# Kernel tuning notes

Measured on AMD Instinct MI355X. Metric: run time of the kernel, lower is better.

The kernel has to match this reference:

```python
import jax, jax.numpy as jnp
import numpy as np

FRACTION = 0.33  # from attn_type='query_selector_0.33'


def setup_inputs() -> dict:
    key = jax.random.key(0)
    k1, k2, k3, k4 = jax.random.split(key, 4)
    B, L, DIM_VAL, DIM_ATTN = 8, 4096, 64, 64
    scale = 1.0 / np.sqrt(DIM_VAL).astype(np.float32)
    x = jax.random.normal(k1, (B, L, DIM_VAL), dtype=jnp.float32)
    Wq = jax.random.normal(k2, (DIM_VAL, DIM_ATTN), dtype=jnp.float32) * scale
    Wk = jax.random.normal(k3, (DIM_VAL, DIM_ATTN), dtype=jnp.float32) * scale
    Wv = jax.random.normal(k4, (DIM_VAL, DIM_VAL), dtype=jnp.float32) * scale
    return {"x": x, "Wq": Wq, "Wk": Wk, "Wv": Wv}


def reference(x, Wq, Wk, Wv):
    # Projections (bias-free Linears)
    Q = jnp.einsum('bld,de->ble', x, Wq)  # [B, L, Da]
    K = jnp.einsum('bld,de->ble', x, Wk)  # [B, L, Da]
    V = jnp.einsum('bld,de->ble', x, Wv)  # [B, L, Dv]

    B, L_Q, Da = Q.shape
    l_Q = int((1.0 - FRACTION) * L_Q)  # static: shapes known at trace time

    # keys.topk(l_Q, dim=1).values -> per-channel top-l_Q along seq; mean over them
    K_top = jax.lax.top_k(jnp.swapaxes(K, 1, 2), l_Q)[0]  # [B, Da, l_Q]
    K_reduce = K_top.mean(axis=-1)                         # [B, Da]

    # score each query against the reduced key; pick top-l_Q queries
    sqk = jnp.einsum('bd,bld->bl', K_reduce, Q)            # [B, L_Q]
    indices = jax.lax.top_k(sqk, l_Q)[1]                   # [B, l_Q] int32

    # gather sampled queries
    Q_sample = jnp.take_along_axis(Q, indices[:, :, None], axis=1)  # [B, l_Q, Da]

    # dense attention for the sampled queries only
    scores = jnp.einsum('bqd,bkd->bqk', Q_sample, K) / jnp.sqrt(jnp.asarray(Da, Q.dtype))
    attn = jax.nn.softmax(scores, axis=-1)                 # [B, l_Q, L]
    out_sel = jnp.einsum('bqk,bkv->bqv', attn, V)          # [B, l_Q, Dv]

    # mean-filled result, scatter attention outputs to selected rows
    mean_values = V.mean(axis=-2)                          # [B, Dv]
    result = jnp.broadcast_to(mean_values[:, None, :], (B, L_Q, V.shape[-1]))
    result = result.at[jnp.arange(B)[:, None], indices].set(out_sel)
    return result
```

## Files before the change

### kernel.cpp

```cpp
#include <hip/hip_runtime.h>
#include <hip/hip_bf16.h>
#include <math.h>

#define BATCH 8
#define SEQ   4096
#define DIM   64
#define LQ    2744
#define QPB   128
#define NQB   22
#define QPAD  2816
#define KS    8
#define L2E   1.4426950408889634f
#define QSC   0.1803368801111204f

typedef _Float16 half8 __attribute__((ext_vector_type(8)));
typedef short    bs8   __attribute__((ext_vector_type(8)));
typedef float    fx16  __attribute__((ext_vector_type(16)));
typedef unsigned short ushort_t;

union UH { uint4 u4; half8 h; };
union UB { unsigned u[4]; uint4 u4; bs8 s; };

__device__ __forceinline__ unsigned pack_bf16(float a, float b) {
    __hip_bfloat162 h = __float22bfloat162_rn(make_float2(a, b));
    union { __hip_bfloat162 h; unsigned u; } cv; cv.h = h; return cv.u;
}

__device__ __forceinline__ unsigned f2sort(float f) {
    unsigned u = __float_as_uint(f);
    return (u & 0x80000000u) ? ~u : (u | 0x80000000u);
}
__device__ __forceinline__ float sort2f(unsigned u) {
    return __uint_as_float((u & 0x80000000u) ? (u & 0x7FFFFFFFu) : ~u);
}

__device__ void radix_select_4096(const unsigned* u, int k, unsigned* hist,
                                  unsigned* wsum, unsigned* res) {
    const int t = threadIdx.x;
    const int lane = t & 63, wv = t >> 6;
    if (t == 0) { res[0] = 0u; res[1] = (unsigned)k; }
    for (int pass = 3; pass >= 0; --pass) {
        const int shift = pass * 8;
        hist[t] = 0u;
        __syncthreads();
        const unsigned pref  = res[0];
        const unsigned kk    = res[1];
        const unsigned hmask = (pass == 3) ? 0u : (0xFFFFFFFFu << (shift + 8));
        for (int i = t; i < 4096; i += 256) {
            unsigned ui = u[i];
            if ((ui & hmask) == pref) atomicAdd(&hist[(ui >> shift) & 255u], 1u);
        }
        __syncthreads();
        const unsigned h = hist[t];
        unsigned s = h;
#pragma unroll
        for (int ofs = 1; ofs < 64; ofs <<= 1) {
            unsigned a = __shfl_down(s, ofs, 64);
            s += (lane + ofs < 64) ? a : 0u;
        }
        if (lane == 0) wsum[wv] = s;
        __syncthreads();
#pragma unroll
        for (int w2 = 0; w2 < 4; ++w2)
            if (w2 > wv) s += wsum[w2];
        if (s >= kk && (s - h) < kk) {
            res[0] = pref | ((unsigned)t << shift);
            res[1] = kk - (s - h);
        }
        __syncthreads();
    }
}

__global__ __launch_bounds__(256) void proj_kernel(
    const float* __restrict__ x,  const float* __restrict__ Wq,
    const float* __restrict__ Wk, const float* __restrict__ Wv,
    float* __restrict__ Q, float* __restrict__ Kt,
    _Float16* __restrict__ Qh, _Float16* __restrict__ Kh,
    ushort_t* __restrict__ Vt, float* __restrict__ pmean) {
    const int rt = blockIdx.x, b = blockIdx.y, t = threadIdx.x;
    __shared__ float4 xs4[64 * 17];
    __shared__ float  red[4][64];
    {
        const float4* xg = (const float4*)(x + ((size_t)b * SEQ + rt * 64) * DIM);
        for (int i = 0; i < 4; ++i) {
            int s = t + 256 * i;
            xs4[(s >> 4) * 17 + (s & 15)] = xg[s];
        }
    }
    __syncthreads();
    const int ch = t & 63, rg = t >> 6;
    float accq[16], acck[16], accv[16];
#pragma unroll
    for (int i = 0; i < 16; ++i) { accq[i] = 0.f; acck[i] = 0.f; accv[i] = 0.f; }
    for (int dc = 0; dc < 4; ++dc) {
        float wq[16], wk[16], wv[16];
#pragma unroll
        for (int dd = 0; dd < 16; ++dd) {
            int d = dc * 16 + dd;
            wq[dd] = Wq[d * 64 + ch]; wk[dd] = Wk[d * 64 + ch]; wv[dd] = Wv[d * 64 + ch];
        }
        for (int r = 0; r < 16; ++r) {
            const int row = rg * 16 + r;
            const float4* xr = &xs4[row * 17 + dc * 4];
            float xv[16];
            float4 a0 = xr[0], a1 = xr[1], a2 = xr[2], a3 = xr[3];
            xv[0]=a0.x; xv[1]=a0.y; xv[2]=a0.z; xv[3]=a0.w;
            xv[4]=a1.x; xv[5]=a1.y; xv[6]=a1.z; xv[7]=a1.w;
            xv[8]=a2.x; xv[9]=a2.y; xv[10]=a2.z; xv[11]=a2.w;
            xv[12]=a3.x; xv[13]=a3.y; xv[14]=a3.z; xv[15]=a3.w;
#pragma unroll
            for (int dd = 0; dd < 16; ++dd) {
                accq[r] = fmaf(xv[dd], wq[dd], accq[r]);
                acck[r] = fmaf(xv[dd], wk[dd], acck[r]);
                accv[r] = fmaf(xv[dd], wv[dd], accv[r]);
            }
        }
    }
    const int rowbase = rt * 64 + rg * 16;
    float sv = 0.f;
#pragma unroll
    for (int r = 0; r < 16; ++r) {
        size_t o = ((size_t)b * SEQ + rowbase + r) * DIM + ch;
        Q[o]  = accq[r];
        Qh[o] = (_Float16)(accq[r] * QSC);
        Kh[o] = (_Float16)acck[r];
        sv += accv[r];
    }
    float4* ktp = (float4*)(Kt + ((size_t)b * 64 + ch) * SEQ + rowbase);
    ktp[0] = make_float4(acck[0], acck[1], acck[2], acck[3]);
    ktp[1] = make_float4(acck[4], acck[5], acck[6], acck[7]);
    ktp[2] = make_float4(acck[8], acck[9], acck[10], acck[11]);
    ktp[3] = make_float4(acck[12], acck[13], acck[14], acck[15]);
    {
        unsigned pk[8];
#pragma unroll
        for (int i = 0; i < 8; ++i) pk[i] = pack_bf16(accv[2*i], accv[2*i+1]);
        uint4* vp = (uint4*)(Vt + ((size_t)(b * 64 + ch)) * SEQ + rowbase);
        vp[0] = make_uint4(pk[0], pk[1], pk[4], pk[5]);
        vp[1] = make_uint4(pk[2], pk[3], pk[6], pk[7]);
    }
    red[rg][ch] = sv;
    __syncthreads();
    if (rg == 0)
        pmean[((size_t)b * 64 + ch) * 64 + rt] =
            red[0][ch] + red[1][ch] + red[2][ch] + red[3][ch];
}

__global__ __launch_bounds__(256) void kmean_kernel(const float* __restrict__ Kt,
                                                    const float* __restrict__ pmean,
                                                    float* __restrict__ Kred,
                                                    float* __restrict__ meanfin) {
    __shared__ unsigned u[4096];
    __shared__ unsigned hist[256];
    __shared__ unsigned wsum[4];
    __shared__ unsigned res[2];
    __shared__ float rsum[4];
    const int bc = blockIdx.x, t = threadIdx.x;
    if (t < 64) {
        float v = pmean[(size_t)bc * 64 + t];
        for (int m = 1; m < 64; m <<= 1) v += __shfl_xor(v, m, 64);
        if (t == 0) meanfin[bc] = v * (1.0f / (float)SEQ);
    }
    const float4* c4 = (const float4*)(Kt + (size_t)bc * SEQ);
    for (int i = t; i < 1024; i += 256) {
        float4 v = c4[i];
        u[i*4+0] = f2sort(v.x); u[i*4+1] = f2sort(v.y);
        u[i*4+2] = f2sort(v.z); u[i*4+3] = f2sort(v.w);
    }
    __syncthreads();
    radix_select_4096(u, LQ, hist, wsum, res);
    const unsigned Tu = res[0];
    const int krem = (int)res[1];
    float loc = 0.f;
    for (int i = t; i < 4096; i += 256)
        if (u[i] > Tu) loc += sort2f(u[i]);
    for (int msk = 1; msk < 64; msk <<= 1) loc += __shfl_xor(loc, msk, 64);
    if ((t & 63) == 0) rsum[t >> 6] = loc;
    __syncthreads();
    if (t == 0) {
        float s = rsum[0] + rsum[1] + rsum[2] + rsum[3] + (float)krem * sort2f(Tu);
        Kred[bc] = s / (float)LQ;
    }
}

__global__ __launch_bounds__(256) void sqk_kernel(const float* __restrict__ Q,
                                                  const float* __restrict__ Kred,
                                                  float* __restrict__ sqk) {
    const int b = blockIdx.y, l = blockIdx.x * 256 + threadIdx.x;
    __shared__ float kr[64];
    if (threadIdx.x < 64) kr[threadIdx.x] = Kred[b * 64 + threadIdx.x];
    __syncthreads();
    const float4* q = (const float4*)(Q + ((size_t)b * SEQ + l) * DIM);
    float s = 0.f;
#pragma unroll
    for (int i = 0; i < 16; ++i) {
        float4 v = q[i];
        s = fmaf(v.x, kr[i*4+0], s); s = fmaf(v.y, kr[i*4+1], s);
        s = fmaf(v.z, kr[i*4+2], s); s = fmaf(v.w, kr[i*4+3], s);
    }
    sqk[b * SEQ + l] = s;
}

__global__ __launch_bounds__(256) void select_kernel(const float* __restrict__ sqk,
                                                     int* __restrict__ sel,
                                                     int* __restrict__ inv) {
    __shared__ unsigned u[4096];
    __shared__ unsigned hist[256];
    __shared__ unsigned wsum[4];
    __shared__ unsigned res[2];
    __shared__ int eq_idx[256];
    __shared__ int cnts[2];
    const int b = blockIdx.x, t = threadIdx.x;
    const float* col = sqk + (size_t)b * SEQ;
    int* invb = inv + (size_t)b * SEQ;
    for (int i = t; i < 4096; i += 256) {
        u[i] = f2sort(col[i]);
        invb[i] = -1;
    }
    if (t < 2) cnts[t] = 0;
    __syncthreads();
    radix_select_4096(u, LQ, hist, wsum, res);
    const unsigned Tu = res[0];
    const int krem = (int)res[1];
    int* selb = sel + b * QPAD;
    for (int i = t; i < 4096; i += 256) {
        unsigned ui = u[i];
        if (ui > Tu) {
            int p = atomicAdd(&cnts[0], 1);
            selb[p] = i;
            invb[i] = p;
        } else if (ui == Tu) {
            int p = atomicAdd(&cnts[1], 1);
            if (p < 256) eq_idx[p] = i;
        }
    }
    __syncthreads();
    if (t == 0) {
        int ng = cnts[0];
        int ne = cnts[1] < 256 ? cnts[1] : 256;
        for (int i = 1; i < ne; ++i) {
            int v = eq_idx[i], j = i - 1;
            while (j >= 0 && eq_idx[j] > v) { eq_idx[j+1] = eq_idx[j]; --j; }
            eq_idx[j+1] = v;
        }
        for (int j = 0; j < krem; ++j) {
            selb[ng + j] = eq_idx[j];
            invb[eq_idx[j]] = ng + j;
        }
    }
    __syncthreads();
    if (t < QPAD - LQ) selb[LQ + t] = selb[LQ - 1];
}

__global__ __launch_bounds__(256, 3) void attn_kernel(
    const ushort_t* __restrict__ Qh, const ushort_t* __restrict__ Kh,
    const ushort_t* __restrict__ Vt, const int* __restrict__ sel,
    float* __restrict__ pl, float* __restrict__ pout) {
    const int lin = blockIdx.x + NQB * (blockIdx.y + KS * blockIdx.z);
    const int ks  = lin & 7;
    const int j8  = lin >> 3;
    const int b   = j8 / NQB;
    const int qt  = j8 % NQB;
    const int t = threadIdx.x, w = t >> 6, lane = t & 63;
    const int col = lane & 31, h = lane >> 5;

    __shared__ ushort_t Ktile[2][32 * 64];
    __shared__ ushort_t Vtile[2][32 * 64];

    half8 qf[4];
    {
        const int q = qt * QPB + w * 32 + col;
        const int row = sel[b * QPAD + q];
        const uint4* qg = (const uint4*)(Qh + ((size_t)b * SEQ + row) * DIM);
#pragma unroll
        for (int m = 0; m < 4; ++m) { UH u; u.u4 = qg[2 * m + h]; qf[m] = u.h; }
    }

    int koff[4], voff[4];
#pragma unroll
    for (int m = 0; m < 4; ++m)
        koff[m] = col * 64 + 8 * ((2 * m + h) ^ (col & 7));
#pragma unroll
    for (int i = 0; i < 4; ++i)
        voff[i] = col * 64 + 8 * ((i * 2 + h) ^ (col & 7));

    fx16 O0, O1;
#pragma unroll
    for (int r = 0; r < 16; ++r) { O0[r] = 0.f; O1[r] = 0.f; }
    float l = 0.f;

    const int srow = t >> 3, sgr = t & 7;
    const int lg = sgr ^ (srow & 7);
    const int vD = lg >> 2, vc = (lg >> 1) & 1, vh = lg & 1;
    const size_t kgbase = ((size_t)b * SEQ + ks * 512 + srow) * DIM + 8 * lg;
    const size_t vgbase = ((size_t)(b * DIM + srow + 32 * vD)) * SEQ
                          + ks * 512 + vc * 16 + vh * 8;

    uint4 kreg = *(const uint4*)(Kh + kgbase);
    uint4 vreg = *(const uint4*)(Vt + vgbase);

    for (int tile = 0; tile < 16; ++tile) {
        const int buf = tile & 1;
        *(uint4*)&Ktile[buf][srow * 64 + sgr * 8] = kreg;
        *(uint4*)&Vtile[buf][srow * 64 + sgr * 8] = vreg;
        __syncthreads();
        if (tile < 15) {
            kreg = *(const uint4*)(Kh + kgbase + (size_t)(tile + 1) * 32 * DIM);
            vreg = *(const uint4*)(Vt + vgbase + (size_t)(tile + 1) * 32);
        }
        fx16 S;
#pragma unroll
        for (int r = 0; r < 16; ++r) S[r] = 0.f;
#pragma unroll
        for (int m = 0; m < 4; ++m) {
            UH kf;
            kf.u4 = *(const uint4*)&Ktile[buf][koff[m]];
            S = __builtin_amdgcn_mfma_f32_32x32x16_f16(kf.h, qf[m], S, 0, 0, 0);
        }
        float p[16];
#pragma unroll
        for (int r = 0; r < 16; ++r) p[r] = exp2f(S[r]);
#pragma unroll
        for (int r = 0; r < 16; ++r) l += p[r];
        UB A0, A1;
#pragma unroll
        for (int v = 0; v < 4; ++v) {
            A0.u[v] = pack_bf16(p[2 * v],     p[2 * v + 1]);
            A1.u[v] = pack_bf16(p[8 + 2 * v], p[8 + 2 * v + 1]);
        }
#pragma unroll
        for (int D = 0; D < 2; ++D) {
            fx16& O = D ? O1 : O0;
#pragma unroll
            for (int c = 0; c < 2; ++c) {
                UB vf;
                vf.u4 = *(const uint4*)&Vtile[buf][voff[D * 2 + c]];
                O = __builtin_amdgcn_mfma_f32_32x32x16_bf16(c ? A1.s : A0.s, vf.s, O, 0, 0, 0);
            }
        }
    }

    l += __shfl_xor(l, 32);

    const int qg0 = qt * QPB + w * 32;
    const size_t base = (size_t)b * QPAD + qg0;
#pragma unroll
    for (int D = 0; D < 2; ++D) {
        const fx16& O = D ? O1 : O0;
#pragma unroll
        for (int r = 0; r < 16; ++r) {
            const int q = (r & 3) + 8 * (r >> 2) + 4 * h;
            atomicAdd(&pout[(base + q) * DIM + D * 32 + col], O[r]);
        }
    }
    if (h == 0) atomicAdd(&pl[base + col], l);
}

__global__ __launch_bounds__(256) void comb_kernel(
    const float* __restrict__ pl, const float* __restrict__ pout,
    const int* __restrict__ inv, const float* __restrict__ meanfin,
    float* __restrict__ out) {
    const int idx = blockIdx.x * 256 + threadIdx.x;
    const int b = idx >> 16;
    const int rc = idx & 65535;
    const int row = rc >> 4, c = rc & 15;
    const int p = inv[b * SEQ + row];
    float4 o;
    if (p >= 0) {
        const size_t s0 = (size_t)b * QPAD + p;
        const float invl = 1.0f / pl[s0];
        float4 a = ((const float4*)(pout + s0 * DIM))[c];
        o = make_float4(a.x * invl, a.y * invl, a.z * invl, a.w * invl);
    } else {
        o = make_float4(meanfin[b * 64 + c * 4 + 0], meanfin[b * 64 + c * 4 + 1],
                        meanfin[b * 64 + c * 4 + 2], meanfin[b * 64 + c * 4 + 3]);
    }
    ((float4*)out)[idx] = o;
}

extern "C" void kernel_launch(void* const* d_in, const int* in_sizes, int n_in,
                              void* d_out, int out_size, void* d_ws, size_t ws_size,
                              hipStream_t stream) {
    const float* x  = (const float*)d_in[0];
    const float* Wq = (const float*)d_in[1];
    const float* Wk = (const float*)d_in[2];
    const float* Wv = (const float*)d_in[3];
    float* out = (float*)d_out;
    char* wsb  = (char*)d_ws;

    float*    Q       = (float*)(wsb);
    _Float16* Qh      = (_Float16*)(wsb + 8388608);
    _Float16* Kh      = (_Float16*)(wsb + 12582912);
    ushort_t* Vt      = (ushort_t*)(wsb + 16777216);
    float*    pmean   = (float*)(wsb + 20971520);
    float*    meanfin = (float*)(wsb + 21102592);
    float*    Kred    = (float*)(wsb + 21104640);
    float*    sqk     = (float*)(wsb + 21106688);
    int*      sel     = (int*)(wsb + 21237760);
    int*      inv     = (int*)(wsb + 21327872);
    float*    Kt      = (float*)(wsb + 21458944);
    float*    pout    = (float*)(wsb + 21458944);
    float*    pl      = (float*)(wsb + 21458944 + 5767168);

    proj_kernel  <<<dim3(64, 8),          256, 0, stream>>>(x, Wq, Wk, Wv, Q, Kt,
                                                            Qh, Kh, Vt, pmean);
    kmean_kernel <<<512,                  256, 0, stream>>>(Kt, pmean, Kred, meanfin);
    sqk_kernel   <<<dim3(16, 8),          256, 0, stream>>>(Q, Kred, sqk);
    select_kernel<<<8,                    256, 0, stream>>>(sqk, sel, inv);
    hipMemsetAsync(pout, 0, 5767168 + 90112, stream);
    attn_kernel  <<<dim3(NQB, KS, BATCH), 256, 0, stream>>>((const ushort_t*)Qh,
                                                            (const ushort_t*)Kh,
                                                            Vt, sel, pl, pout);
    comb_kernel  <<<2048,                 256, 0, stream>>>(pl, pout, inv, meanfin, out);
}
```

Measured before the change: 195.5 us.

## Trim radix passes, fuse memset into sqk, widen attention K tiles, scalar x loads

The projection kernel drops its LDS staging of x and reads each row through wave-uniform (readfirstlane) global loads. The key top-k mean now runs only two 8-bit radix passes and approximates values in the threshold bucket by the bucket midpoint. The pout/pl zeroing moves out of a separate memset and into the sqk kernel. The attention kernel processes 64-key tiles per barrier with two prefetched loads, raises the waves-per-EU launch bound to 4, and wraps the MFMA groups in s_setprio. The radix change trades exactness of K_reduce for fewer passes, and the larger tiles double the LDS per block.

Result: faster. 187.8 us (-3.9%).

```diff
diff --git a/kernel.cpp b/kernel.cpp
--- a/kernel.cpp
+++ b/kernel.cpp
@@ -35,11 +35,11 @@
 }
 
 __device__ void radix_select_4096(const unsigned* u, int k, unsigned* hist,
-                                  unsigned* wsum, unsigned* res) {
+                                  unsigned* wsum, unsigned* res, int pass_lo) {
     const int t = threadIdx.x;
     const int lane = t & 63, wv = t >> 6;
     if (t == 0) { res[0] = 0u; res[1] = (unsigned)k; }
-    for (int pass = 3; pass >= 0; --pass) {
+    for (int pass = 3; pass >= pass_lo; --pass) {
         const int shift = pass * 8;
         hist[t] = 0u;
         __syncthreads();
@@ -78,17 +78,9 @@
     _Float16* __restrict__ Qh, _Float16* __restrict__ Kh,
     ushort_t* __restrict__ Vt, float* __restrict__ pmean) {
     const int rt = blockIdx.x, b = blockIdx.y, t = threadIdx.x;
-    __shared__ float4 xs4[64 * 17];
     __shared__ float  red[4][64];
-    {
-        const float4* xg = (const float4*)(x + ((size_t)b * SEQ + rt * 64) * DIM);
-        for (int i = 0; i < 4; ++i) {
-            int s = t + 256 * i;
-            xs4[(s >> 4) * 17 + (s & 15)] = xg[s];
-        }
-    }
-    __syncthreads();
     const int ch = t & 63, rg = t >> 6;
+    const float* xb = x + (size_t)b * SEQ * DIM;
     float accq[16], acck[16], accv[16];
 #pragma unroll
     for (int i = 0; i < 16; ++i) { accq[i] = 0.f; acck[i] = 0.f; accv[i] = 0.f; }
@@ -100,14 +92,12 @@
             wq[dd] = Wq[d * 64 + ch]; wk[dd] = Wk[d * 64 + ch]; wv[dd] = Wv[d * 64 + ch];
         }
         for (int r = 0; r < 16; ++r) {
-            const int row = rg * 16 + r;
-            const float4* xr = &xs4[row * 17 + dc * 4];
+            const int off = (rt * 64 + rg * 16 + r) * DIM + dc * 16;
+            const float* xrow =
+                xb + (unsigned)__builtin_amdgcn_readfirstlane(off);
             float xv[16];
-            float4 a0 = xr[0], a1 = xr[1], a2 = xr[2], a3 = xr[3];
-            xv[0]=a0.x; xv[1]=a0.y; xv[2]=a0.z; xv[3]=a0.w;
-            xv[4]=a1.x; xv[5]=a1.y; xv[6]=a1.z; xv[7]=a1.w;
-            xv[8]=a2.x; xv[9]=a2.y; xv[10]=a2.z; xv[11]=a2.w;
-            xv[12]=a3.x; xv[13]=a3.y; xv[14]=a3.z; xv[15]=a3.w;
+#pragma unroll
+            for (int dd = 0; dd < 16; ++dd) xv[dd] = xrow[dd];
 #pragma unroll
             for (int dd = 0; dd < 16; ++dd) {
                 accq[r] = fmaf(xv[dd], wq[dd], accq[r]);
@@ -168,27 +158,34 @@
         u[i*4+2] = f2sort(v.z); u[i*4+3] = f2sort(v.w);
     }
     __syncthreads();
-    radix_select_4096(u, LQ, hist, wsum, res);
+    radix_select_4096(u, LQ, hist, wsum, res, 2);
     const unsigned Tu = res[0];
     const int krem = (int)res[1];
     float loc = 0.f;
     for (int i = t; i < 4096; i += 256)
-        if (u[i] > Tu) loc += sort2f(u[i]);
+        if ((u[i] & 0xFFFF0000u) > Tu) loc += sort2f(u[i]);
     for (int msk = 1; msk < 64; msk <<= 1) loc += __shfl_xor(loc, msk, 64);
     if ((t & 63) == 0) rsum[t >> 6] = loc;
     __syncthreads();
     if (t == 0) {
-        float s = rsum[0] + rsum[1] + rsum[2] + rsum[3] + (float)krem * sort2f(Tu);
+        float s = rsum[0] + rsum[1] + rsum[2] + rsum[3]
+                + (float)krem * sort2f(Tu | 0x8000u);
         Kred[bc] = s / (float)LQ;
     }
 }
 
 __global__ __launch_bounds__(256) void sqk_kernel(const float* __restrict__ Q,
                                                   const float* __restrict__ Kred,
-                                                  float* __restrict__ sqk) {
+                                                  float* __restrict__ sqk,
+                                                  float4* __restrict__ pz) {
     const int b = blockIdx.y, l = blockIdx.x * 256 + threadIdx.x;
     __shared__ float kr[64];
     if (threadIdx.x < 64) kr[threadIdx.x] = Kred[b * 64 + threadIdx.x];
+    {
+        const int tid = (blockIdx.y * 16 + blockIdx.x) * 256 + threadIdx.x;
+        const float4 z = make_float4(0.f, 0.f, 0.f, 0.f);
+        for (int i = tid; i < 366080; i += 32768) pz[i] = z;
+    }
     __syncthreads();
     const float4* q = (const float4*)(Q + ((size_t)b * SEQ + l) * DIM);
     float s = 0.f;
@@ -219,7 +216,7 @@
     }
     if (t < 2) cnts[t] = 0;
     __syncthreads();
-    radix_select_4096(u, LQ, hist, wsum, res);
+    radix_select_4096(u, LQ, hist, wsum, res, 0);
     const unsigned Tu = res[0];
     const int krem = (int)res[1];
     int* selb = sel + b * QPAD;
@@ -252,7 +249,7 @@
     if (t < QPAD - LQ) selb[LQ + t] = selb[LQ - 1];
 }
 
-__global__ __launch_bounds__(256, 3) void attn_kernel(
+__global__ __launch_bounds__(256, 4) void attn_kernel(
     const ushort_t* __restrict__ Qh, const ushort_t* __restrict__ Kh,
     const ushort_t* __restrict__ Vt, const int* __restrict__ sel,
     float* __restrict__ pl, float* __restrict__ pout) {
@@ -264,8 +261,8 @@
     const int t = threadIdx.x, w = t >> 6, lane = t & 63;
     const int col = lane & 31, h = lane >> 5;
 
-    __shared__ ushort_t Ktile[2][32 * 64];
-    __shared__ ushort_t Vtile[2][32 * 64];
+    __shared__ ushort_t Ktile[2][64 * 64];
+    __shared__ ushort_t Vtile[2][2 * 32 * 64];
 
     half8 qf[4];
     {
@@ -296,48 +293,66 @@
     const size_t vgbase = ((size_t)(b * DIM + srow + 32 * vD)) * SEQ
                           + ks * 512 + vc * 16 + vh * 8;
 
-    uint4 kreg = *(const uint4*)(Kh + kgbase);
-    uint4 vreg = *(const uint4*)(Vt + vgbase);
-
-    for (int tile = 0; tile < 16; ++tile) {
+    uint4 kreg0 = *(const uint4*)(Kh + kgbase);
+    uint4 kreg1 = *(const uint4*)(Kh + kgbase + 32 * DIM);
+    uint4 vreg0 = *(const uint4*)(Vt + vgbase);
+    uint4 vreg1 = *(const uint4*)(Vt + vgbase + 32);
+
+    for (int tile = 0; tile < 8; ++tile) {
         const int buf = tile & 1;
-        *(uint4*)&Ktile[buf][srow * 64 + sgr * 8] = kreg;
-        *(uint4*)&Vtile[buf][srow * 64 + sgr * 8] = vreg;
-        __syncthreads();
-        if (tile < 15) {
-            kreg = *(const uint4*)(Kh + kgbase + (size_t)(tile + 1) * 32 * DIM);
-            vreg = *(const uint4*)(Vt + vgbase + (size_t)(tile + 1) * 32);
-        }
-        fx16 S;
-#pragma unroll
-        for (int r = 0; r < 16; ++r) S[r] = 0.f;
-#pragma unroll
-        for (int m = 0; m < 4; ++m) {
-            UH kf;
-            kf.u4 = *(const uint4*)&Ktile[buf][koff[m]];
-            S = __builtin_amdgcn_mfma_f32_32x32x16_f16(kf.h, qf[m], S, 0, 0, 0);
-        }
-        float p[16];
-#pragma unroll
-        for (int r = 0; r < 16; ++r) p[r] = exp2f(S[r]);
-#pragma unroll
-        for (int r = 0; r < 16; ++r) l += p[r];
-        UB A0, A1;
-#pragma unroll
-        for (int v = 0; v < 4; ++v) {
-            A0.u[v] = pack_bf16(p[2 * v],     p[2 * v + 1]);
-            A1.u[v] = pack_bf16(p[8 + 2 * v], p[8 + 2 * v + 1]);
-        }
-#pragma unroll
-        for (int D = 0; D < 2; ++D) {
-            fx16& O = D ? O1 : O0;
-#pragma unroll
-            for (int c = 0; c < 2; ++c) {
-                UB vf;
-                vf.u4 = *(const uint4*)&Vtile[buf][voff[D * 2 + c]];
-                O = __builtin_amdgcn_mfma_f32_32x32x16_bf16(c ? A1.s : A0.s, vf.s, O, 0, 0, 0);
+        *(uint4*)&Ktile[buf][srow * 64 + sgr * 8]          = kreg0;
+        *(uint4*)&Ktile[buf][(srow + 32) * 64 + sgr * 8]   = kreg1;
+        *(uint4*)&Vtile[buf][srow * 64 + sgr * 8]          = vreg0;
+        *(uint4*)&Vtile[buf][2048 + srow * 64 + sgr * 8]   = vreg1;
+        __syncthreads();
+        if (tile < 7) {
+            const size_t ko = kgbase + (size_t)(tile + 1) * 64 * DIM;
+            const size_t vo = vgbase + (size_t)(tile + 1) * 64;
+            kreg0 = *(const uint4*)(Kh + ko);
+            kreg1 = *(const uint4*)(Kh + ko + 32 * DIM);
+            vreg0 = *(const uint4*)(Vt + vo);
+            vreg1 = *(const uint4*)(Vt + vo + 32);
+        }
+#pragma unroll
+        for (int ss = 0; ss < 2; ++ss) {
+            const int so = ss * 2048;
+            fx16 S;
+#pragma unroll
+            for (int r = 0; r < 16; ++r) S[r] = 0.f;
+            __builtin_amdgcn_s_setprio(1);
+#pragma unroll
+            for (int m = 0; m < 4; ++m) {
+                UH kf;
+                kf.u4 = *(const uint4*)&Ktile[buf][koff[m] + so];
+                S = __builtin_amdgcn_mfma_f32_32x32x16_f16(kf.h, qf[m], S, 0, 0, 0);
             }
-        }
+            __builtin_amdgcn_s_setprio(0);
+            float p[16];
+#pragma unroll
+            for (int r = 0; r < 16; ++r) p[r] = exp2f(S[r]);
+#pragma unroll
+            for (int r = 0; r < 16; ++r) l += p[r];
+            UB A0, A1;
+#pragma unroll
+            for (int v = 0; v < 4; ++v) {
+                A0.u[v] = pack_bf16(p[2 * v],     p[2 * v + 1]);
+                A1.u[v] = pack_bf16(p[8 + 2 * v], p[8 + 2 * v + 1]);
+            }
+            __builtin_amdgcn_s_setprio(1);
+#pragma unroll
+            for (int D = 0; D < 2; ++D) {
+                fx16& O = D ? O1 : O0;
+#pragma unroll
+                for (int c = 0; c < 2; ++c) {
+                    UB vf;
+                    vf.u4 = *(const uint4*)&Vtile[buf][voff[D * 2 + c] + so];
+                    O = __builtin_amdgcn_mfma_f32_32x32x16_bf16(
+                            c ? A1.s : A0.s, vf.s, O, 0, 0, 0);
+                }
+            }
+            __builtin_amdgcn_s_setprio(0);
+        }
+        __syncthreads();
     }
 
     l += __shfl_xor(l, 32);
@@ -405,9 +420,9 @@
     proj_kernel  <<<dim3(64, 8),          256, 0, stream>>>(x, Wq, Wk, Wv, Q, Kt,
                                                             Qh, Kh, Vt, pmean);
     kmean_kernel <<<512,                  256, 0, stream>>>(Kt, pmean, Kred, meanfin);
-    sqk_kernel   <<<dim3(16, 8),          256, 0, stream>>>(Q, Kred, sqk);
+    sqk_kernel   <<<dim3(16, 8),          256, 0, stream>>>(Q, Kred, sqk,
+                                                            (float4*)pout);
     select_kernel<<<8,                    256, 0, stream>>>(sqk, sel, inv);
-    hipMemsetAsync(pout, 0, 5767168 + 90112, stream);
     attn_kernel  <<<dim3(NQB, KS, BATCH), 256, 0, stream>>>((const ushort_t*)Qh,
                                                             (const ushort_t*)Kh,
                                                             Vt, sel, pl, pout);
```
